# Kernel tuning notes

Hardware: AMD Instinct MI355X
Metric: run time of the kernel (lower is better)

Reference implementation:

```python
import jax, jax.numpy as jnp
import numpy as np

EPS = 1e-5
MAX_NORM = 1.0 - 1e-4

def _artanh(x):
    x = jnp.clip(x, -1.0 + 1e-5, 1.0 - 1e-5)
    return 0.5 * (jnp.log1p(x) - jnp.log1p(-x))

def _norm(x):
    return jnp.sqrt(jnp.maximum(jnp.sum(x * x, axis=-1, keepdims=True), EPS * EPS))

def _project(x):
    # clip points into the Poincare ball (c=1)
    n = _norm(x)
    return x * jnp.minimum(1.0, MAX_NORM / n)

def _logmap0(x):
    n = _norm(x)
    return _artanh(n) * x / n

def _expmap0(v):
    n = _norm(v)
    return jnp.tanh(n) * v / n

def _mobius_add(x, y):
    x2 = jnp.sum(x * x, -1, keepdims=True)
    y2 = jnp.sum(y * y, -1, keepdims=True)
    xy = jnp.sum(x * y, -1, keepdims=True)
    num = (1.0 + 2.0 * xy + y2) * x + (1.0 - x2) * y
    den = 1.0 + 2.0 * xy + x2 * y2
    return num / jnp.maximum(den, EPS)

def _mobius_matvec_all(W, x):
    # x: [B,T,D] on ball, W: [K,D,D] -> [B,T,K,D] (mx = x @ W[k].T for each expert k)
    mx = jnp.einsum('btd,ked->btke', x, W)
    xn = _norm(x)[:, :, None, :]            # [B,T,1,1]
    mn = _norm(mx)                          # [B,T,K,1]
    return jnp.tanh(mn / xn * _artanh(xn)) * mx / mn

def _depthwise_conv1d(x, w, b):
    # x: [B,T,C], w: [C,1,3] depthwise, padding=1
    y = jax.lax.conv_general_dilated(
        jnp.transpose(x, (0, 2, 1)), w, (1,), 'SAME',
        feature_group_count=x.shape[-1],
        dimension_numbers=('NCW', 'OIW', 'NCW'))
    return jnp.transpose(y, (0, 2, 1)) + b

def setup_inputs() -> dict:
    key = jax.random.key(0)
    ks = jax.random.split(key, 10)
    B, T, V, D, K, E, R = 8, 512, 50257, 64, 17, 32, 40
    return {
        'tokens': jax.random.randint(ks[0], (B, T), 0, V),
        'token_embed': 0.02 * jax.random.normal(ks[1], (V, D), jnp.float32),
        'conv_w': 0.3 * jax.random.normal(ks[2], (D, 1, 3), jnp.float32),
        'conv_b': jnp.zeros((D,), jnp.float32),
        'lin_w': 0.1 * jax.random.normal(ks[3], (D, K), jnp.float32),
        'lin_b': jnp.zeros((K,), jnp.float32),
        'exp_W': (1.0 / 8.0) * jax.random.normal(ks[4], (K, D, D), jnp.float32),
        'exp_bias': 0.01 * jax.random.normal(ks[5], (K, D), jnp.float32),
        'ln_gamma': jnp.ones((K, E), jnp.float32),
        'ln_beta': jnp.zeros((K, E), jnp.float32),
        'rel_T': jax.random.normal(ks[6], (R, E, E), jnp.float32),
        'rel_S': jax.random.normal(ks[7], (R, E, E), jnp.float32),
    }

def reference(tokens, token_embed, conv_w, conv_b, lin_w, lin_b,
              exp_W, exp_bias, ln_gamma, ln_beta, rel_T, rel_S):
    B, T = tokens.shape
    h0 = token_embed[tokens]                                  # [B,T,64]
    # TinyPosRouter: depthwise conv -> linear -> log_softmax
    hc = _depthwise_conv1d(h0, conv_w, conv_b)
    logp = jax.nn.log_softmax(hc @ lin_w + lin_b, axis=-1)    # [B,T,17]
    p = jnp.exp(logp)
    # round-trip through tangent space (as in source)
    x = _expmap0(_logmap0(_project(h0)))                      # [B,T,64]
    # all 17 hyperbolic experts, batched
    mv = _mobius_matvec_all(exp_W, x)                         # [B,T,17,64]
    y = _project(_mobius_add(mv, _project(exp_bias)))         # mobius bias add
    yt = _logmap0(y)                                          # tangent [B,T,17,64]
    a, g = jnp.split(yt, 2, axis=-1)
    y_glu = a * jax.nn.sigmoid(g)                             # [B,T,17,32]
    mu = jnp.mean(y_glu, -1, keepdims=True)
    var = jnp.var(y_glu, -1, keepdims=True)
    y_ln = (y_glu - mu) / jnp.sqrt(var + 1e-5) * ln_gamma + ln_beta
    y_out = _expmap0(y_ln)                                    # [B,T,17,32]
    y_avg = jnp.einsum('btke,btk->bte', y_out, p)             # soft routing
    # per-relation biaffine scores
    Th = jnp.einsum('btd,rde->brte', y_avg, rel_T)            # [B,40,T,32]
    Sd = jnp.einsum('btd,rde->brte', y_avg, rel_S)
    scores = jnp.einsum('brid,brjd->brij', Th, Sd) / Th.shape[-1]  # [B,40,T,T]
    score_rel = jnp.max(scores, axis=1)                       # [B,T,T]
    score_rel = jnp.where(jnp.eye(T, dtype=bool)[None], -1e9, score_rel)
    # greedy arborescence approximation: each dependent picks max-scoring head
    tree = jnp.argmax(score_rel, axis=1)                      # [B,T]
    return tree, score_rel, logp
```

## Files before the change

kernel.cpp:

```cpp
#include <hip/hip_runtime.h>
#include <hip/hip_bf16.h>
#include <math.h>

#define EPS   1e-5f
#define EPS2  (1e-5f * 1e-5f)
#define MAXN  (1.0f - 1e-4f)

typedef __attribute__((ext_vector_type(8))) short bf16x8;
typedef __attribute__((ext_vector_type(4))) float f32x4;

__device__ __forceinline__ float artanh_(float x) {
    x = fminf(fmaxf(x, -1.0f + 1e-5f), 1.0f - 1e-5f);
    return 0.5f * (log1pf(x) - log1pf(-x));
}
__device__ __forceinline__ float redw(float v) {
    #pragma unroll
    for (int m = 32; m >= 1; m >>= 1) v += __shfl_xor(v, m);
    return v;
}
__device__ __forceinline__ float red16(float v) {
    v += __shfl_xor(v, 1); v += __shfl_xor(v, 2);
    v += __shfl_xor(v, 4); v += __shfl_xor(v, 8);
    return v;
}
__device__ __forceinline__ float red8(float v) {
    v += __shfl_xor(v, 1); v += __shfl_xor(v, 2); v += __shfl_xor(v, 4);
    return v;
}
__device__ __forceinline__ float sigmoid_(float z) { return 1.0f / (1.0f + expf(-z)); }
__device__ __forceinline__ ushort f2bf(float f) {
    union { __hip_bfloat16 b; ushort u; } cv;
    cv.b = __float2bfloat16(f);
    return cv.u;
}
__device__ __forceinline__ bf16x8 pack8(float4 lo, float4 hi) {
    bf16x8 r;
    r[0] = (short)f2bf(lo.x); r[1] = (short)f2bf(lo.y);
    r[2] = (short)f2bf(lo.z); r[3] = (short)f2bf(lo.w);
    r[4] = (short)f2bf(hi.x); r[5] = (short)f2bf(hi.y);
    r[6] = (short)f2bf(hi.z); r[7] = (short)f2bf(hi.w);
    return r;
}

__global__ __launch_bounds__(64) void k1_token(
    const int* __restrict__ tokens, const float* __restrict__ emb,
    const float* __restrict__ conv_w, const float* __restrict__ conv_b,
    const float* __restrict__ lin_w, const float* __restrict__ lin_b,
    float* __restrict__ x_out, float* __restrict__ xn_out,
    float* __restrict__ p_out, float* __restrict__ logp_out)
{
    const int tok = blockIdx.x;
    const int t   = tok & 511;
    const int c   = threadIdx.x;

    const int id0 = tokens[tok];
    float h0 = emb[id0 * 64 + c];
    float hm = 0.0f, hp = 0.0f;
    if (t > 0)   hm = emb[tokens[tok - 1] * 64 + c];
    if (t < 511) hp = emb[tokens[tok + 1] * 64 + c];

    float hc = conv_w[c * 3 + 0] * hm + conv_w[c * 3 + 1] * h0 +
               conv_w[c * 3 + 2] * hp + conv_b[c];

    __shared__ float lg[17];
    #pragma unroll
    for (int j = 0; j < 17; ++j) {
        float v = redw(hc * lin_w[c * 17 + j]);
        if (c == 0) lg[j] = v + lin_b[j];
    }
    __syncthreads();
    float mx = -1e30f;
    #pragma unroll
    for (int j = 0; j < 17; ++j) mx = fmaxf(mx, lg[j]);
    float se = 0.0f;
    #pragma unroll
    for (int j = 0; j < 17; ++j) se += expf(lg[j] - mx);
    float lse = logf(se);
    if (c < 17) {
        float lp = lg[c] - mx - lse;
        logp_out[tok * 17 + c] = lp;
        p_out[tok * 17 + c]    = expf(lp);
    }

    float n0 = sqrtf(fmaxf(redw(h0 * h0), EPS2));
    float xp = h0 * fminf(1.0f, MAXN / n0);
    float n1 = sqrtf(fmaxf(redw(xp * xp), EPS2));
    float v1 = artanh_(n1) / n1 * xp;
    float n2 = sqrtf(fmaxf(redw(v1 * v1), EPS2));
    float xv = tanhf(n2) / n2 * v1;

    x_out[tok * 64 + c] = xv;
    float n3 = sqrtf(fmaxf(redw(xv * xv), EPS2));
    if (c == 0) xn_out[tok] = n3;
}

__global__ __launch_bounds__(256) void k2_expert(
    const float* __restrict__ x_in, const float* __restrict__ xn_in,
    const float* __restrict__ p_in, const float* __restrict__ expW,
    const float* __restrict__ expB, const float* __restrict__ g_in,
    const float* __restrict__ b_in, __hip_bfloat16* __restrict__ yk_out)
{
    __shared__ float mv_s[16][65];
    __shared__ float pb[64];
    __shared__ float gsk[32], bsk[32];
    __shared__ float p_sk[16];
    __shared__ float xn_s[16], axn_s[16];
    __shared__ float y2s_s;

    const int tid = threadIdx.x;
    const int l = tid & 63, w = tid >> 6;
    const int tg = tid >> 4, eg = tid & 15;
    const int k = blockIdx.x >> 8;
    const int chunk = blockIdx.x & 255;
    const int tok0 = chunk * 16;

    {
        const int d0 = (l >> 4) * 8;
        const float* ap = x_in + (tok0 + (l & 15)) * 64 + d0;
        const float* bp = expW + k * 4096 + (16 * w + (l & 15)) * 64 + d0;
        bf16x8 a0 = pack8(*reinterpret_cast<const float4*>(ap),
                          *reinterpret_cast<const float4*>(ap + 4));
        bf16x8 a1 = pack8(*reinterpret_cast<const float4*>(ap + 32),
                          *reinterpret_cast<const float4*>(ap + 36));
        bf16x8 b0 = pack8(*reinterpret_cast<const float4*>(bp),
                          *reinterpret_cast<const float4*>(bp + 4));
        bf16x8 b1 = pack8(*reinterpret_cast<const float4*>(bp + 32),
                          *reinterpret_cast<const float4*>(bp + 36));
        f32x4 acc = {0.f, 0.f, 0.f, 0.f};
        acc = __builtin_amdgcn_mfma_f32_16x16x32_bf16(a0, b0, acc, 0, 0, 0);
        acc = __builtin_amdgcn_mfma_f32_16x16x32_bf16(a1, b1, acc, 0, 0, 0);
        #pragma unroll
        for (int q = 0; q < 4; ++q)
            mv_s[(l >> 4) * 4 + q][16 * w + (l & 15)] = acc[q];
    }

    if (tid < 64) {
        float wv = expB[k * 64 + tid];
        float s = redw(wv * wv);
        float n = sqrtf(fmaxf(s, EPS2));
        float sc = fminf(1.0f, MAXN / n);
        pb[tid] = wv * sc;
        if (tid == 0) y2s_s = s * sc * sc;
    }
    if (tid >= 64 && tid < 96)  gsk[tid - 64] = g_in[k * 32 + (tid - 64)];
    if (tid >= 96 && tid < 128) bsk[tid - 96] = b_in[k * 32 + (tid - 96)];
    if (tid >= 128 && tid < 144) p_sk[tid - 128] = p_in[(tok0 + tid - 128) * 17 + k];
    if (tid >= 144 && tid < 160) {
        float xn = xn_in[tok0 + tid - 144];
        xn_s[tid - 144] = xn;
        axn_s[tid - 144] = artanh_(xn);
    }
    __syncthreads();

    const float xnv = xn_s[tg], axnv = axn_s[tg];
    float4 mvq = *reinterpret_cast<const float4*>(&mv_s[tg][eg * 4]);
    float mv0 = mvq.x, mv1 = mvq.y, mv2 = mvq.z, mv3 = mvq.w;

    float mn = sqrtf(fmaxf(red16(mv0*mv0 + mv1*mv1 + mv2*mv2 + mv3*mv3), EPS2));
    float tv = tanhf(mn / xnv * axnv);
    float cf = tv / mn;
    float xa0 = cf * mv0, xa1 = cf * mv1, xa2 = cf * mv2, xa3 = cf * mv3;
    float x2 = tv * tv;

    float4 pbv = *reinterpret_cast<const float4*>(&pb[eg * 4]);
    float xy = red16(xa0*pbv.x + xa1*pbv.y + xa2*pbv.z + xa3*pbv.w);
    float y2 = y2s_s;
    float ca = 1.0f + 2.0f * xy + y2;
    float cb = 1.0f - x2;
    float den = fmaxf(1.0f + 2.0f * xy + x2 * y2, EPS);
    float rden = 1.0f / den;
    float y0 = (ca * xa0 + cb * pbv.x) * rden;
    float y1 = (ca * xa1 + cb * pbv.y) * rden;
    float y2c = (ca * xa2 + cb * pbv.z) * rden;
    float y3 = (ca * xa3 + cb * pbv.w) * rden;

    float s2 = red16(y0*y0 + y1*y1 + y2c*y2c + y3*y3);
    float nP = sqrtf(fmaxf(s2, EPS2));
    float scP = fminf(1.0f, MAXN / nP);
    y0 *= scP; y1 *= scP; y2c *= scP; y3 *= scP;

    float n2 = sqrtf(fmaxf(s2 * scP * scP, EPS2));
    float lc = artanh_(n2) / n2;
    float yt0 = lc * y0, yt1 = lc * y1, yt2 = lc * y2c, yt3 = lc * y3;

    float pr0 = __shfl_xor(yt0, 8), pr1 = __shfl_xor(yt1, 8);
    float pr2 = __shfl_xor(yt2, 8), pr3 = __shfl_xor(yt3, 8);
    float gl0, gl1, gl2, gl3;
    if (eg < 8) {
        gl0 = yt0 * sigmoid_(pr0); gl1 = yt1 * sigmoid_(pr1);
        gl2 = yt2 * sigmoid_(pr2); gl3 = yt3 * sigmoid_(pr3);
    } else {
        gl0 = pr0 * sigmoid_(yt0); gl1 = pr1 * sigmoid_(yt1);
        gl2 = pr2 * sigmoid_(yt2); gl3 = pr3 * sigmoid_(yt3);
    }

    float mu = red8(gl0 + gl1 + gl2 + gl3) * (1.0f / 32.0f);
    float sq = red8(gl0*gl0 + gl1*gl1 + gl2*gl2 + gl3*gl3) * (1.0f / 32.0f);
    float rstd = rsqrtf(fmaxf(sq - mu * mu, 0.0f) + 1e-5f);
    int c0 = 4 * (eg & 7);
    float ln0 = (gl0 - mu) * rstd * gsk[c0 + 0] + bsk[c0 + 0];
    float ln1 = (gl1 - mu) * rstd * gsk[c0 + 1] + bsk[c0 + 1];
    float ln2 = (gl2 - mu) * rstd * gsk[c0 + 2] + bsk[c0 + 2];
    float ln3 = (gl3 - mu) * rstd * gsk[c0 + 3] + bsk[c0 + 3];

    float n3 = sqrtf(fmaxf(red8(ln0*ln0 + ln1*ln1 + ln2*ln2 + ln3*ln3), EPS2));
    float tc = tanhf(n3) / n3;

    float pk = p_sk[tg];
    float wq = pk * tc;

    if (eg < 8) {
        int tok = tok0 + tg;
        ushort4 o;
        o.x = f2bf(wq * ln0);
        o.y = f2bf(wq * ln1);
        o.z = f2bf(wq * ln2);
        o.w = f2bf(wq * ln3);
        *reinterpret_cast<ushort4*>(
            reinterpret_cast<ushort*>(yk_out) + ((size_t)tok * 17 + k) * 32 + c0) = o;
    }
}

__global__ __launch_bounds__(256) void k3_reduce(
    const __hip_bfloat16* __restrict__ yk, ushort* __restrict__ yab)
{
    int idx = blockIdx.x * 256 + threadIdx.x;
    int tok = idx >> 5, e = idx & 31;
    const __hip_bfloat16* p = yk + (size_t)tok * 17 * 32 + e;
    float s = 0.0f;
    #pragma unroll
    for (int k = 0; k < 17; ++k) s += __bfloat162float(p[k * 32]);
    yab[idx] = f2bf(s);
}

__global__ __launch_bounds__(256) void k4_rel(
    const ushort* __restrict__ yab, const float* __restrict__ relT,
    const float* __restrict__ relS, ushort* __restrict__ Z)
{
    const int blk = blockIdx.x;
    const int b = blk / 160;
    const int rem = blk % 160;
    const int r = rem >> 2, tq = rem & 3;
    __shared__ float Ts[32][33], Ss[32][33], Mm[32][33];
    __shared__ float Zb[128][33];
    const int tid = threadIdx.x;
    const int l = tid & 63, w = tid >> 6;

    {
        int d = tid >> 3, e0 = (tid & 7) * 4;
        float4 wT = *reinterpret_cast<const float4*>(&relT[r * 1024 + tid * 4]);
        float4 wS = *reinterpret_cast<const float4*>(&relS[r * 1024 + tid * 4]);
        Ts[d][e0 + 0] = wT.x; Ts[d][e0 + 1] = wT.y;
        Ts[d][e0 + 2] = wT.z; Ts[d][e0 + 3] = wT.w;
        Ss[d][e0 + 0] = wS.x; Ss[d][e0 + 1] = wS.y;
        Ss[d][e0 + 2] = wS.z; Ss[d][e0 + 3] = wS.w;
    }
    __syncthreads();

    {
        int d = tid >> 3, dp0 = (tid & 7) * 4;
        float m0 = 0.f, m1 = 0.f, m2 = 0.f, m3 = 0.f;
        #pragma unroll
        for (int e = 0; e < 32; ++e) {
            float tvv = Ts[d][e];
            m0 = fmaf(tvv, Ss[dp0 + 0][e], m0);
            m1 = fmaf(tvv, Ss[dp0 + 1][e], m1);
            m2 = fmaf(tvv, Ss[dp0 + 2][e], m2);
            m3 = fmaf(tvv, Ss[dp0 + 3][e], m3);
        }
        Mm[d][dp0 + 0] = m0; Mm[d][dp0 + 1] = m1;
        Mm[d][dp0 + 2] = m2; Mm[d][dp0 + 3] = m3;
    }
    __syncthreads();

    bf16x8 bm0, bm1;
    #pragma unroll
    for (int i = 0; i < 8; ++i) {
        int d = (l >> 4) * 8 + i;
        bm0[i] = (short)f2bf(Mm[d][(l & 15)]);
        bm1[i] = (short)f2bf(Mm[d][16 + (l & 15)]);
    }

    #pragma unroll
    for (int s = 0; s < 2; ++s) {
        int trow = tq * 128 + (w * 2 + s) * 16 + (l & 15);
        bf16x8 a = *reinterpret_cast<const bf16x8*>(
            yab + ((size_t)(b * 512) + trow) * 32 + (l >> 4) * 8);
        f32x4 acc0 = {0.f, 0.f, 0.f, 0.f}, acc1 = {0.f, 0.f, 0.f, 0.f};
        acc0 = __builtin_amdgcn_mfma_f32_16x16x32_bf16(a, bm0, acc0, 0, 0, 0);
        acc1 = __builtin_amdgcn_mfma_f32_16x16x32_bf16(a, bm1, acc1, 0, 0, 0);
        #pragma unroll
        for (int q = 0; q < 4; ++q) {
            int lr = (w * 2 + s) * 16 + (l >> 4) * 4 + q;
            Zb[lr][(l & 15)]      = acc0[q];
            Zb[lr][16 + (l & 15)] = acc1[q];
        }
    }
    __syncthreads();

    {
        int t2 = tid >> 1, half = tid & 1;
        union { ushort u[16]; uint4 q[2]; } pk;
        #pragma unroll
        for (int j = 0; j < 16; ++j) pk.u[j] = f2bf(Zb[t2][half * 16 + j]);
        size_t off = ((size_t)(b * 40 + r) * 512 + tq * 128 + t2) * 32 + half * 16;
        *reinterpret_cast<uint4*>(Z + off)     = pk.q[0];
        *reinterpret_cast<uint4*>(Z + off + 8) = pk.q[1];
    }
}

__global__ __launch_bounds__(1024) void k5_scores(
    const ushort* __restrict__ Z, const ushort* __restrict__ yab,
    float* __restrict__ score_out)
{
    __shared__ float L[4][64][64];

    const int blk = blockIdx.x;
    const int b = blk >> 6, tile = blk & 63;
    const int it = (tile >> 3) * 64, jt = (tile & 7) * 64;
    const int w = threadIdx.x >> 6, lane = threadIdx.x & 63;
    const int q = w >> 2, s = w & 3;
    const int i0 = it + s * 16;
    const int arow = i0 + (lane & 15);
    const int koff = (lane >> 4) * 8;

    bf16x8 bb[4];
    #pragma unroll
    for (int c = 0; c < 4; ++c) {
        int jrow = jt + c * 16 + (lane & 15);
        bb[c] = *reinterpret_cast<const bf16x8*>(
            yab + ((size_t)(b * 512) + jrow) * 32 + koff);
    }

    f32x4 runmax[4];
    #pragma unroll
    for (int c = 0; c < 4; ++c)
        #pragma unroll
        for (int qq = 0; qq < 4; ++qq) runmax[c][qq] = -3.0e38f;

    const int r0 = q * 10;
    #pragma unroll 2
    for (int r = r0; r < r0 + 10; ++r) {
        bf16x8 a = *reinterpret_cast<const bf16x8*>(
            Z + ((size_t)(b * 40 + r) * 512 + arow) * 32 + koff);
        #pragma unroll
        for (int c = 0; c < 4; ++c) {
            f32x4 acc = {0.f, 0.f, 0.f, 0.f};
            acc = __builtin_amdgcn_mfma_f32_16x16x32_bf16(a, bb[c], acc, 0, 0, 0);
            #pragma unroll
            for (int qq = 0; qq < 4; ++qq) runmax[c][qq] = fmaxf(runmax[c][qq], acc[qq]);
        }
    }

    #pragma unroll
    for (int c = 0; c < 4; ++c) {
        #pragma unroll
        for (int qq = 0; qq < 4; ++qq) {
            int li = s * 16 + (lane >> 4) * 4 + qq;
            int lj = c * 16 + (lane & 15);
            L[q][li][lj] = runmax[c][qq];
        }
    }
    __syncthreads();

    #pragma unroll
    for (int idx = threadIdx.x; idx < 4096; idx += 1024) {
        int i = idx >> 6, j = idx & 63;
        float v = fmaxf(fmaxf(L[0][i][j], L[1][i][j]),
                        fmaxf(L[2][i][j], L[3][i][j])) * (1.0f / 32.0f);
        int gi = it + i, gj = jt + j;
        if (gi == gj) v = -1e9f;
        score_out[((size_t)b * 512 + gi) * 512 + gj] = v;
    }
}

__global__ __launch_bounds__(256) void k6_argmax(
    const float* __restrict__ score, float* __restrict__ tree)
{
    __shared__ float vals[16][17];
    __shared__ int   idxs[16][17];
    const int b  = blockIdx.x >> 5;
    const int jc = blockIdx.x & 31;
    const int jl = threadIdx.x & 15, ic = threadIdx.x >> 4;
    const int j = jc * 16 + jl;
    const float* S = score + (size_t)b * 512 * 512 + j;
    const int i0 = ic * 32;
    float best = -3.0e38f; int bi = i0;
    #pragma unroll 8
    for (int qq = 0; qq < 32; ++qq) {
        float v = S[(size_t)(i0 + qq) * 512];
        if (v > best) { best = v; bi = i0 + qq; }
    }
    vals[ic][jl] = best;
    idxs[ic][jl] = bi;
    __syncthreads();
    if (threadIdx.x < 16) {
        const int jj = threadIdx.x;
        float bv = vals[0][jj]; int bidx = idxs[0][jj];
        #pragma unroll
        for (int ic2 = 1; ic2 < 16; ++ic2) {
            float v = vals[ic2][jj];
            if (v > bv) { bv = v; bidx = idxs[ic2][jj]; }
        }
        tree[b * 512 + jc * 16 + jj] = (float)bidx;
    }
}

extern "C" void kernel_launch(void* const* d_in, const int* in_sizes, int n_in,
                              void* d_out, int out_size, void* d_ws, size_t ws_size,
                              hipStream_t stream)
{
    const int*   tokens  = (const int*)  d_in[0];
    const float* emb     = (const float*)d_in[1];
    const float* conv_w  = (const float*)d_in[2];
    const float* conv_b  = (const float*)d_in[3];
    const float* lin_w   = (const float*)d_in[4];
    const float* lin_b   = (const float*)d_in[5];
    const float* expW    = (const float*)d_in[6];
    const float* expB    = (const float*)d_in[7];
    const float* ln_g    = (const float*)d_in[8];
    const float* ln_b    = (const float*)d_in[9];
    const float* relT    = (const float*)d_in[10];
    const float* relS    = (const float*)d_in[11];

    float* out = (float*)d_out;
    float* tree_out  = out;
    float* score_out = out + 4096;
    float* logp_out  = out + 4096 + 2097152;

    float* ws = (float*)d_ws;
    float* x_ws  = ws;
    float* xn_ws = ws + 262144;
    float* p_ws  = ws + 266240;
    ushort* yab_ws = (ushort*)(ws + 335872);
    __hip_bfloat16* yk_ws = (__hip_bfloat16*)(ws + 401408);
    ushort* Z_ws = (ushort*)(ws + 1515520);

    k1_token<<<4096, 64, 0, stream>>>(tokens, emb, conv_w, conv_b, lin_w, lin_b,
                                      x_ws, xn_ws, p_ws, logp_out);
    k2_expert<<<4352, 256, 0, stream>>>(x_ws, xn_ws, p_ws, expW, expB, ln_g, ln_b, yk_ws);
    k3_reduce<<<512, 256, 0, stream>>>(yk_ws, yab_ws);
    k4_rel<<<1280, 256, 0, stream>>>(yab_ws, relT, relS, Z_ws);
    k5_scores<<<512, 1024, 0, stream>>>(Z_ws, yab_ws, score_out);
    k6_argmax<<<256, 256, 0, stream>>>(score_out, tree_out);
}
```

Before: 74.43 us.

## Fuse expert reduction via atomics and fold argmax into score kernel

The per-expert bf16 staging buffer and its separate reduce kernel are replaced by fp32 atomicAdd into a zeroed per-token accumulator, which k1 initialises. The score kernel now computes a per-column partial argmax, packed as an ordered key plus index, and merges it with 64-bit atomicMax. A tiny kernel then decodes the tree indices, so the full score tensor no longer has to be re-read. The router softmax also moves from shared memory to shuffles. The cost is atomic contention of 17 experts per element, non-deterministic fp32 summation order, and extra conversion of fp32 inputs to bf16 inside k4 and k5.

```diff
diff --git a/kernel.cpp b/kernel.cpp
--- a/kernel.cpp
+++ b/kernel.cpp
@@ -47,7 +47,8 @@
     const float* __restrict__ conv_w, const float* __restrict__ conv_b,
     const float* __restrict__ lin_w, const float* __restrict__ lin_b,
     float* __restrict__ x_out, float* __restrict__ xn_out,
-    float* __restrict__ p_out, float* __restrict__ logp_out)
+    float* __restrict__ p_out, float* __restrict__ logp_out,
+    float* __restrict__ ya)
 {
     const int tok = blockIdx.x;
     const int t   = tok & 511;
@@ -62,25 +63,24 @@
     float hc = conv_w[c * 3 + 0] * hm + conv_w[c * 3 + 1] * h0 +
                conv_w[c * 3 + 2] * hp + conv_b[c];
 
-    __shared__ float lg[17];
+    float myLg = 0.0f;
     #pragma unroll
     for (int j = 0; j < 17; ++j) {
         float v = redw(hc * lin_w[c * 17 + j]);
-        if (c == 0) lg[j] = v + lin_b[j];
-    }
-    __syncthreads();
-    float mx = -1e30f;
-    #pragma unroll
-    for (int j = 0; j < 17; ++j) mx = fmaxf(mx, lg[j]);
-    float se = 0.0f;
-    #pragma unroll
-    for (int j = 0; j < 17; ++j) se += expf(lg[j] - mx);
+        if (c == j) myLg = v + lin_b[j];
+    }
+    float mx = (c < 17) ? myLg : -1e30f;
+    #pragma unroll
+    for (int m = 32; m >= 1; m >>= 1) mx = fmaxf(mx, __shfl_xor(mx, m));
+    float ev = (c < 17) ? expf(myLg - mx) : 0.0f;
+    float se = redw(ev);
     float lse = logf(se);
     if (c < 17) {
-        float lp = lg[c] - mx - lse;
+        float lp = myLg - mx - lse;
         logp_out[tok * 17 + c] = lp;
         p_out[tok * 17 + c]    = expf(lp);
     }
+    if (c < 32) ya[(size_t)tok * 32 + c] = 0.0f;
 
     float n0 = sqrtf(fmaxf(redw(h0 * h0), EPS2));
     float xp = h0 * fminf(1.0f, MAXN / n0);
@@ -98,7 +98,7 @@
     const float* __restrict__ x_in, const float* __restrict__ xn_in,
     const float* __restrict__ p_in, const float* __restrict__ expW,
     const float* __restrict__ expB, const float* __restrict__ g_in,
-    const float* __restrict__ b_in, __hip_bfloat16* __restrict__ yk_out)
+    const float* __restrict__ b_in, float* __restrict__ ya)
 {
     __shared__ float mv_s[16][65];
     __shared__ float pb[64];
@@ -210,32 +210,18 @@
     float wq = pk * tc;
 
     if (eg < 8) {
-        int tok = tok0 + tg;
-        ushort4 o;
-        o.x = f2bf(wq * ln0);
-        o.y = f2bf(wq * ln1);
-        o.z = f2bf(wq * ln2);
-        o.w = f2bf(wq * ln3);
-        *reinterpret_cast<ushort4*>(
-            reinterpret_cast<ushort*>(yk_out) + ((size_t)tok * 17 + k) * 32 + c0) = o;
-    }
-}
-
-__global__ __launch_bounds__(256) void k3_reduce(
-    const __hip_bfloat16* __restrict__ yk, ushort* __restrict__ yab)
-{
-    int idx = blockIdx.x * 256 + threadIdx.x;
-    int tok = idx >> 5, e = idx & 31;
-    const __hip_bfloat16* p = yk + (size_t)tok * 17 * 32 + e;
-    float s = 0.0f;
-    #pragma unroll
-    for (int k = 0; k < 17; ++k) s += __bfloat162float(p[k * 32]);
-    yab[idx] = f2bf(s);
+        float* dst = ya + (size_t)(tok0 + tg) * 32 + c0;
+        atomicAdd(dst + 0, wq * ln0);
+        atomicAdd(dst + 1, wq * ln1);
+        atomicAdd(dst + 2, wq * ln2);
+        atomicAdd(dst + 3, wq * ln3);
+    }
 }
 
 __global__ __launch_bounds__(256) void k4_rel(
-    const ushort* __restrict__ yab, const float* __restrict__ relT,
-    const float* __restrict__ relS, ushort* __restrict__ Z)
+    const float* __restrict__ ya, const float* __restrict__ relT,
+    const float* __restrict__ relS, ushort* __restrict__ Z,
+    unsigned long long* __restrict__ pmax)
 {
     const int blk = blockIdx.x;
     const int b = blk / 160;
@@ -246,6 +232,9 @@
     const int tid = threadIdx.x;
     const int l = tid & 63, w = tid >> 6;
 
+    if (r == 0 && tid < 128)
+        pmax[(size_t)b * 512 + tq * 128 + tid] = 0ull;
+
     {
         int d = tid >> 3, e0 = (tid & 7) * 4;
         float4 wT = *reinterpret_cast<const float4*>(&relT[r * 1024 + tid * 4]);
@@ -284,8 +273,9 @@
     #pragma unroll
     for (int s = 0; s < 2; ++s) {
         int trow = tq * 128 + (w * 2 + s) * 16 + (l & 15);
-        bf16x8 a = *reinterpret_cast<const bf16x8*>(
-            yab + ((size_t)(b * 512) + trow) * 32 + (l >> 4) * 8);
+        const float* yp = ya + ((size_t)(b * 512) + trow) * 32 + (l >> 4) * 8;
+        bf16x8 a = pack8(*reinterpret_cast<const float4*>(yp),
+                         *reinterpret_cast<const float4*>(yp + 4));
         f32x4 acc0 = {0.f, 0.f, 0.f, 0.f}, acc1 = {0.f, 0.f, 0.f, 0.f};
         acc0 = __builtin_amdgcn_mfma_f32_16x16x32_bf16(a, bm0, acc0, 0, 0, 0);
         acc1 = __builtin_amdgcn_mfma_f32_16x16x32_bf16(a, bm1, acc1, 0, 0, 0);
@@ -310,10 +300,11 @@
 }
 
 __global__ __launch_bounds__(1024) void k5_scores(
-    const ushort* __restrict__ Z, const ushort* __restrict__ yab,
-    float* __restrict__ score_out)
+    const ushort* __restrict__ Z, const float* __restrict__ ya,
+    float* __restrict__ score_out, unsigned long long* __restrict__ pmax)
 {
     __shared__ float L[4][64][64];
+    __shared__ unsigned long long pk_s[16][64];
 
     const int blk = blockIdx.x;
     const int b = blk >> 6, tile = blk & 63;
@@ -328,8 +319,9 @@
     #pragma unroll
     for (int c = 0; c < 4; ++c) {
         int jrow = jt + c * 16 + (lane & 15);
-        bb[c] = *reinterpret_cast<const bf16x8*>(
-            yab + ((size_t)(b * 512) + jrow) * 32 + koff);
+        const float* yp = ya + ((size_t)(b * 512) + jrow) * 32 + koff;
+        bb[c] = pack8(*reinterpret_cast<const float4*>(yp),
+                      *reinterpret_cast<const float4*>(yp + 4));
     }
 
     f32x4 runmax[4];
@@ -363,47 +355,41 @@
     }
     __syncthreads();
 
-    #pragma unroll
-    for (int idx = threadIdx.x; idx < 4096; idx += 1024) {
-        int i = idx >> 6, j = idx & 63;
-        float v = fmaxf(fmaxf(L[0][i][j], L[1][i][j]),
-                        fmaxf(L[2][i][j], L[3][i][j])) * (1.0f / 32.0f);
-        int gi = it + i, gj = jt + j;
-        if (gi == gj) v = -1e9f;
-        score_out[((size_t)b * 512 + gi) * 512 + gj] = v;
-    }
-}
-
-__global__ __launch_bounds__(256) void k6_argmax(
-    const float* __restrict__ score, float* __restrict__ tree)
-{
-    __shared__ float vals[16][17];
-    __shared__ int   idxs[16][17];
-    const int b  = blockIdx.x >> 5;
-    const int jc = blockIdx.x & 31;
-    const int jl = threadIdx.x & 15, ic = threadIdx.x >> 4;
-    const int j = jc * 16 + jl;
-    const float* S = score + (size_t)b * 512 * 512 + j;
-    const int i0 = ic * 32;
-    float best = -3.0e38f; int bi = i0;
-    #pragma unroll 8
-    for (int qq = 0; qq < 32; ++qq) {
-        float v = S[(size_t)(i0 + qq) * 512];
-        if (v > best) { best = v; bi = i0 + qq; }
-    }
-    vals[ic][jl] = best;
-    idxs[ic][jl] = bi;
-    __syncthreads();
-    if (threadIdx.x < 16) {
-        const int jj = threadIdx.x;
-        float bv = vals[0][jj]; int bidx = idxs[0][jj];
-        #pragma unroll
-        for (int ic2 = 1; ic2 < 16; ++ic2) {
-            float v = vals[ic2][jj];
-            if (v > bv) { bv = v; bidx = idxs[ic2][jj]; }
-        }
-        tree[b * 512 + jc * 16 + jj] = (float)bidx;
-    }
+    {
+        const int jl = threadIdx.x & 63, ig = threadIdx.x >> 6;
+        const int gj = jt + jl;
+        float bestv = -3.0e38f; int besti = it;
+        #pragma unroll
+        for (int p = 0; p < 4; ++p) {
+            int i = ig + p * 16;
+            float v = fmaxf(fmaxf(L[0][i][jl], L[1][i][jl]),
+                            fmaxf(L[2][i][jl], L[3][i][jl])) * (1.0f / 32.0f);
+            int gi = it + i;
+            if (gi == gj) v = -1e9f;
+            score_out[((size_t)b * 512 + gi) * 512 + gj] = v;
+            if (v > bestv) { bestv = v; besti = gi; }
+        }
+        unsigned int ub = __float_as_uint(bestv);
+        unsigned int ok = (ub >> 31) ? ~ub : (ub | 0x80000000u);
+        pk_s[ig][jl] = ((unsigned long long)ok << 32) | (unsigned int)(511 - besti);
+    }
+    __syncthreads();
+    if (threadIdx.x < 64) {
+        unsigned long long best = pk_s[0][threadIdx.x];
+        #pragma unroll
+        for (int g = 1; g < 16; ++g) {
+            unsigned long long v = pk_s[g][threadIdx.x];
+            if (v > best) best = v;
+        }
+        atomicMax(&pmax[(size_t)b * 512 + jt + threadIdx.x], best);
+    }
+}
+
+__global__ __launch_bounds__(256) void k6_tree(
+    const unsigned long long* __restrict__ pmax, float* __restrict__ tree)
+{
+    int idx = blockIdx.x * 256 + threadIdx.x;
+    tree[idx] = (float)(511 - (int)(pmax[idx] & 0x1ffull));
 }
 
 extern "C" void kernel_launch(void* const* d_in, const int* in_sizes, int n_in,
@@ -432,15 +418,15 @@
     float* x_ws  = ws;
     float* xn_ws = ws + 262144;
     float* p_ws  = ws + 266240;
-    ushort* yab_ws = (ushort*)(ws + 335872);
-    __hip_bfloat16* yk_ws = (__hip_bfloat16*)(ws + 401408);
-    ushort* Z_ws = (ushort*)(ws + 1515520);
+    float* ya_ws = ws + 335872;
+    ushort* Z_ws = (ushort*)(ws + 466944);
+    unsigned long long* pmax_ws =
+        (unsigned long long*)(ws + 3088384);
 
     k1_token<<<4096, 64, 0, stream>>>(tokens, emb, conv_w, conv_b, lin_w, lin_b,
-                                      x_ws, xn_ws, p_ws, logp_out);
-    k2_expert<<<4352, 256, 0, stream>>>(x_ws, xn_ws, p_ws, expW, expB, ln_g, ln_b, yk_ws);
-    k3_reduce<<<512, 256, 0, stream>>>(yk_ws, yab_ws);
-    k4_rel<<<1280, 256, 0, stream>>>(yab_ws, relT, relS, Z_ws);
-    k5_scores<<<512, 1024, 0, stream>>>(Z_ws, yab_ws, score_out);
-    k6_argmax<<<256, 256, 0, stream>>>(score_out, tree_out);
-}
+                                      x_ws, xn_ws, p_ws, logp_out, ya_ws);
+    k2_expert<<<4352, 256, 0, stream>>>(x_ws, xn_ws, p_ws, expW, expB, ln_g, ln_b, ya_ws);
+    k4_rel<<<1280, 256, 0, stream>>>(ya_ws, relT, relS, Z_ws, pmax_ws);
+    k5_scores<<<512, 1024, 0, stream>>>(Z_ws, ya_ws, score_out, pmax_ws);
+    k6_tree<<<16, 256, 0, stream>>>(pmax_ws, tree_out);
+}
```

New measurement: 83.15 us. 1.12x slower.
